# Kernel tuning notes

Measured on AMD Instinct MI355X. Metric: run time of the kernel, lower is better.

The kernel has to match this reference:

```python
import jax, jax.numpy as jnp
import numpy as np

D_MODEL = 1024
N_HEADS = 16
HEAD_DIM = D_MODEL // N_HEADS


def setup_inputs() -> dict:
    key = jax.random.key(0)
    ks = jax.random.split(key, 5)
    B, T = 2, 2048
    x = jax.random.normal(ks[0], (B, T, D_MODEL), dtype=jnp.float32)
    s = 1.0 / np.sqrt(D_MODEL)
    qkv_w = jax.random.uniform(ks[1], (3 * D_MODEL, D_MODEL), jnp.float32, -s, s)
    qkv_b = jax.random.uniform(ks[2], (3 * D_MODEL,), jnp.float32, -s, s)
    out_w = jax.random.uniform(ks[3], (D_MODEL, D_MODEL), jnp.float32, -s, s)
    out_b = jax.random.uniform(ks[4], (D_MODEL,), jnp.float32, -s, s)
    return {"x": x, "qkv_w": qkv_w, "qkv_b": qkv_b, "out_w": out_w, "out_b": out_b}


def reference(x, qkv_w, qkv_b, out_w, out_b):
    B, T, _ = x.shape
    # qkv projection: [B,T,3*D]
    qkv = x @ qkv_w.T + qkv_b
    qkv = qkv.reshape(B, T, 3, N_HEADS, HEAD_DIM)
    qkv = jnp.transpose(qkv, (2, 0, 3, 1, 4))  # [3,B,H,T,Hd]
    q, k, v = qkv[0], qkv[1], qkv[2]
    scale = 1.0 / np.sqrt(HEAD_DIM)
    scores = jnp.einsum("bhqd,bhkd->bhqk", q, k) * scale  # [B,H,T,T]
    causal = jnp.tril(jnp.ones((T, T), dtype=bool))
    scores = jnp.where(causal, scores, -jnp.inf)
    weights = jax.nn.softmax(scores, axis=-1)
    # dropout in eval mode (identity)
    out = jnp.einsum("bhqk,bhkd->bhqd", weights, v)  # [B,H,T,Hd]
    out = jnp.transpose(out, (0, 2, 1, 3)).reshape(B, T, D_MODEL)
    return out @ out_w.T + out_b
```

## Files before the change

### kernel.cpp

```cpp
#include <hip/hip_runtime.h>
#include <hip/hip_bf16.h>


typedef __bf16 bf16;
typedef bf16 bf16x8 __attribute__((ext_vector_type(8)));
typedef bf16 bf16x4 __attribute__((ext_vector_type(4)));
typedef float f32x4 __attribute__((ext_vector_type(4)));

#define MFMA16(a, b, c) __builtin_amdgcn_mfma_f32_16x16x32_bf16((a), (b), (c), 0, 0, 0)

static constexpr int D_MODEL = 1024;
static constexpr int NH = 16;
static constexpr int HD = 64;
static constexpr int SEQ = 2048;
static constexpr int NB = 2;
static constexpr float QSCALE = 0.125f * 1.44269504088896340736f;

__device__ __forceinline__ bf16x8 cvt8(const float* p) {
    float4 u0 = *(const float4*)p;
    float4 u1 = *(const float4*)(p + 4);
    bf16x8 v = { (bf16)u0.x, (bf16)u0.y, (bf16)u0.z, (bf16)u0.w,
                 (bf16)u1.x, (bf16)u1.y, (bf16)u1.z, (bf16)u1.w };
    return v;
}

__device__ __forceinline__ void async16(const bf16* g, bf16* l) {
    __builtin_amdgcn_global_load_lds(
        (const __attribute__((address_space(1))) void*)g,
        (__attribute__((address_space(3))) void*)l, 16, 0, 0);
}

__global__ __launch_bounds__(256)
void k_cast(const float* __restrict__ in, bf16* __restrict__ out, int n8)
{
    int i = blockIdx.x * 256 + threadIdx.x;
    if (i < n8) *(bf16x8*)&out[(size_t)i * 8] = cvt8(&in[(size_t)i * 8]);
}

__global__ __launch_bounds__(256)
void k_qkv(const bf16* __restrict__ x, const bf16* __restrict__ w,
           const float* __restrict__ bias,
           bf16* __restrict__ Qb, bf16* __restrict__ Kb, bf16* __restrict__ VbT)
{
    __shared__ bf16 As[128 * 32];
    __shared__ bf16 Ws[128 * 32];

    const int tid  = threadIdx.x;
    const int wv   = tid >> 6;
    const int lane = tid & 63;
    const int lr   = lane & 15;
    const int lk   = lane >> 4;
    const int wm   = wv >> 1, wn = wv & 1;
    const int m0   = blockIdx.x * 128;
    const int n0   = blockIdx.y * 128;

    const int sRow = tid >> 2;
    const int sCol = (tid & 3) * 8;
    const int sOff = sRow * 32 + sCol;

    f32x4 acc[4][4] = {};

    for (int kt = 0; kt < 1024; kt += 32) {
        __syncthreads();
        async16(&x[(size_t)(m0 + sRow     ) * 1024 + kt + sCol], &As[sOff]);
        async16(&x[(size_t)(m0 + 64 + sRow) * 1024 + kt + sCol], &As[64 * 32 + sOff]);
        async16(&w[(size_t)(n0 + sRow     ) * 1024 + kt + sCol], &Ws[sOff]);
        async16(&w[(size_t)(n0 + 64 + sRow) * 1024 + kt + sCol], &Ws[64 * 32 + sOff]);
        __syncthreads();

        bf16x8 a[4], b[4];
        #pragma unroll
        for (int i = 0; i < 4; i++) {
            a[i] = *(const bf16x8*)&As[(wm * 64 + i * 16 + lr) * 32 + lk * 8];
            b[i] = *(const bf16x8*)&Ws[(wn * 64 + i * 16 + lr) * 32 + lk * 8];
        }
        #pragma unroll
        for (int i = 0; i < 4; i++)
            #pragma unroll
            for (int j = 0; j < 4; j++)
                acc[i][j] = MFMA16(a[i], b[j], acc[i][j]);
    }

    #pragma unroll
    for (int i = 0; i < 4; i++) {
        #pragma unroll
        for (int j = 0; j < 4; j++) {
            const int gm0 = m0 + wm * 64 + i * 16 + lk * 4;
            const int gn  = n0 + wn * 64 + j * 16 + lr;
            const int sel = gn >> 10;
            const int rem = gn & 1023;
            const int h   = rem >> 6;
            const int hd  = rem & 63;
            const int bb  = gm0 >> 11;
            const int t0  = gm0 & 2047;
            if (sel == 2) {
                bf16x4 p;
                #pragma unroll
                for (int r = 0; r < 4; r++) p[r] = (bf16)(acc[i][j][r] + bias[gn]);
                *(bf16x4*)&VbT[((size_t)(bb * NH + h) * HD + hd) * SEQ + t0] = p;
            } else {
                #pragma unroll
                for (int r = 0; r < 4; r++) {
                    float v = acc[i][j][r] + bias[gn];
                    size_t idx = ((size_t)(bb * NH + h) * SEQ + t0 + r) * HD + hd;
                    if (sel == 0) Qb[idx] = (bf16)(v * QSCALE);
                    else          Kb[idx] = (bf16)v;
                }
            }
        }
    }
}

__global__ __launch_bounds__(256)
void k_attn(const bf16* __restrict__ Qb, const bf16* __restrict__ Kb,
            const bf16* __restrict__ VbT, bf16* __restrict__ AO)
{
    __shared__ bf16 Ks[2][64 * 64];
    __shared__ bf16 Vt[2][64 * 64];
    __shared__ bf16 Ps[64 * 64];

    const int tid  = threadIdx.x;
    const int wv   = tid >> 6;
    const int lane = tid & 63;
    const int lr   = lane & 15;
    const int lk   = lane >> 4;
    const int bh   = blockIdx.y;
    const int qt   = ((bh >> 3) & 1) ? (31 - (int)blockIdx.x) : (int)blockIdx.x;

    const bf16* Qp  = Qb  + (size_t)bh * SEQ * HD;
    const bf16* Kp  = Kb  + (size_t)bh * SEQ * HD;
    const bf16* Vtp = VbT + (size_t)bh * HD * SEQ;

    const int qg = qt * 64 + wv * 16 + lr;

    bf16x8 qf[2];
    qf[0] = *(const bf16x8*)&Qp[(size_t)qg * HD +      lk * 8];
    qf[1] = *(const bf16x8*)&Qp[(size_t)qg * HD + 32 + lk * 8];

    f32x4 ot[4] = {};
    float lsum = 0.f;

    const int srow   = tid >> 3;
    const int sgcol  = ((tid & 7) ^ (srow & 7)) * 8;
    const int sldse  = tid * 8;
    const int swz    = lr & 7;

    auto stage = [&](int buf, int k0) {
        async16(&Kp [(size_t)(k0 + srow     ) * HD  + sgcol], &Ks[buf][       sldse]);
        async16(&Kp [(size_t)(k0 + 32 + srow) * HD  + sgcol], &Ks[buf][2048 + sldse]);
        async16(&Vtp[(size_t)(srow          ) * SEQ + k0 + sgcol], &Vt[buf][       sldse]);
        async16(&Vtp[(size_t)(32 + srow     ) * SEQ + k0 + sgcol], &Vt[buf][2048 + sldse]);
    };

    stage(0, 0);

    for (int kt = 0; kt <= qt; kt++) {
        const int p = kt & 1;
        if (kt < qt) {
            stage(p ^ 1, (kt + 1) * 64);
            asm volatile("s_waitcnt vmcnt(4)" ::: "memory");
        } else {
            asm volatile("s_waitcnt vmcnt(0)" ::: "memory");
        }
        __builtin_amdgcn_s_barrier();

        f32x4 s[4] = {};
        #pragma unroll
        for (int j = 0; j < 4; j++) {
            #pragma unroll
            for (int c = 0; c < 2; c++) {
                bf16x8 ka = *(const bf16x8*)
                    &Ks[p][(j * 16 + lr) * 64 + (((4 * c + lk) ^ swz) << 3)];
                s[j] = MFMA16(ka, qf[c], s[j]);
            }
        }

        const int k0 = kt * 64;
        const bool diag = (kt == qt);
        #pragma unroll
        for (int j = 0; j < 4; j++) {
            const int keyb = k0 + j * 16 + lk * 4;
            f32x4 pv;
            #pragma unroll
            for (int r = 0; r < 4; r++) {
                float e = __builtin_amdgcn_exp2f(s[j][r]);
                if (diag) e = (keyb + r > qg) ? 0.f : e;
                pv[r] = e;
            }
            s[j] = pv;
            lsum += (pv[0] + pv[1]) + (pv[2] + pv[3]);
        }

        #pragma unroll
        for (int j = 0; j < 4; j++) {
            bf16x4 p4 = { (bf16)s[j][0], (bf16)s[j][1], (bf16)s[j][2], (bf16)s[j][3] };
            *(bf16x4*)&Ps[(wv * 16 + lr) * 64 +
                          (((2 * j + (lk >> 1)) ^ swz) << 3) + ((lk & 1) << 2)] = p4;
        }

        #pragma unroll
        for (int c = 0; c < 2; c++) {
            bf16x8 pb = *(const bf16x8*)
                &Ps[(wv * 16 + lr) * 64 + (((4 * c + lk) ^ swz) << 3)];
            #pragma unroll
            for (int jh = 0; jh < 4; jh++) {
                bf16x8 va = *(const bf16x8*)
                    &Vt[p][(jh * 16 + lr) * 64 + (((4 * c + lk) ^ swz) << 3)];
                ot[jh] = MFMA16(va, pb, ot[jh]);
            }
        }

        asm volatile("" ::: "memory");
        __builtin_amdgcn_s_barrier();
    }

    lsum += __shfl_xor(lsum, 16);
    lsum += __shfl_xor(lsum, 32);

    const float inv = 1.0f / lsum;
    const int b_ = bh >> 4, h_ = bh & 15;
    const size_t base = ((size_t)(b_ * SEQ + qg)) * D_MODEL + h_ * HD;
    #pragma unroll
    for (int jh = 0; jh < 4; jh++) {
        bf16x4 o4 = { (bf16)(ot[jh][0] * inv), (bf16)(ot[jh][1] * inv),
                      (bf16)(ot[jh][2] * inv), (bf16)(ot[jh][3] * inv) };
        *(bf16x4*)&AO[base + jh * 16 + lk * 4] = o4;
    }
}

__global__ __launch_bounds__(256)
void k_oproj(const bf16* __restrict__ a_, const bf16* __restrict__ w,
             const float* __restrict__ bias, float* __restrict__ out)
{
    __shared__ bf16 As[128 * 32];
    __shared__ bf16 Ws[64 * 32];

    const int tid  = threadIdx.x;
    const int wv   = tid >> 6;
    const int lane = tid & 63;
    const int lr   = lane & 15;
    const int lk   = lane >> 4;
    const int wm   = wv >> 1, wn = wv & 1;
    const int m0   = blockIdx.x * 128;
    const int n0   = blockIdx.y * 64;

    const int sRow = tid >> 2;
    const int sCol = (tid & 3) * 8;
    const int sOff = sRow * 32 + sCol;

    f32x4 acc[4][2] = {};

    for (int kt = 0; kt < 1024; kt += 32) {
        __syncthreads();
        async16(&a_[(size_t)(m0 + sRow     ) * 1024 + kt + sCol], &As[sOff]);
        async16(&a_[(size_t)(m0 + 64 + sRow) * 1024 + kt + sCol], &As[64 * 32 + sOff]);
        async16(&w [(size_t)(n0 + sRow     ) * 1024 + kt + sCol], &Ws[sOff]);
        __syncthreads();

        bf16x8 a[4], b[2];
        #pragma unroll
        for (int i = 0; i < 4; i++)
            a[i] = *(const bf16x8*)&As[(wm * 64 + i * 16 + lr) * 32 + lk * 8];
        #pragma unroll
        for (int j = 0; j < 2; j++)
            b[j] = *(const bf16x8*)&Ws[(wn * 32 + j * 16 + lr) * 32 + lk * 8];
        #pragma unroll
        for (int i = 0; i < 4; i++)
            #pragma unroll
            for (int j = 0; j < 2; j++)
                acc[i][j] = MFMA16(a[i], b[j], acc[i][j]);
    }

    #pragma unroll
    for (int i = 0; i < 4; i++) {
        #pragma unroll
        for (int j = 0; j < 2; j++) {
            #pragma unroll
            for (int r = 0; r < 4; r++) {
                int gm = m0 + wm * 64 + i * 16 + lk * 4 + r;
                int gn = n0 + wn * 32 + j * 16 + lr;
                out[(size_t)gm * 1024 + gn] = acc[i][j][r] + bias[gn];
            }
        }
    }
}

extern "C" void kernel_launch(void* const* d_in, const int* in_sizes, int n_in,
                              void* d_out, int out_size, void* d_ws, size_t ws_size,
                              hipStream_t stream)
{
    const float* x     = (const float*)d_in[0];
    const float* qkv_w = (const float*)d_in[1];
    const float* qkv_b = (const float*)d_in[2];
    const float* out_w = (const float*)d_in[3];
    const float* out_b = (const float*)d_in[4];
    float* out = (float*)d_out;

    const size_t SZ = (size_t)NB * NH * SEQ * HD;
    bf16* Qb  = (bf16*)d_ws;
    bf16* Kb  = Qb + SZ;
    bf16* VbT = Kb + SZ;
    bf16* AO  = VbT + SZ;
    bf16* xb  = AO + SZ;
    bf16* wqb = xb + SZ;
    bf16* wob = wqb + (size_t)3 * D_MODEL * D_MODEL;

    hipLaunchKernelGGL(k_cast, dim3(2048), dim3(256), 0, stream, x,     xb,  524288);
    hipLaunchKernelGGL(k_cast, dim3(1536), dim3(256), 0, stream, qkv_w, wqb, 393216);
    hipLaunchKernelGGL(k_cast, dim3(512),  dim3(256), 0, stream, out_w, wob, 131072);

    hipLaunchKernelGGL(k_qkv, dim3(32, 24), dim3(256), 0, stream,
                       xb, wqb, qkv_b, Qb, Kb, VbT);
    hipLaunchKernelGGL(k_attn, dim3(32, 32), dim3(256), 0, stream,
                       Qb, Kb, VbT, AO);
    hipLaunchKernelGGL(k_oproj, dim3(32, 16), dim3(256), 0, stream,
                       AO, wob, out_b, out);
}
```

Before: 176.2 us.

## Double-buffer LDS tiles in QKV and output projection GEMMs

Both projection GEMMs now use two LDS buffers. The next K-slice is fetched with async global-to-LDS loads while MFMAs run on the current slice, and partial vmcnt waits let only the older loads drain. This is meant to hide global load latency that the previous load-sync-compute loop exposed. It doubles LDS use per block, which may reduce occupancy, and it relies on hand-placed waitcnt and barrier for correctness.

```diff
diff --git a/kernel.cpp b/kernel.cpp
--- a/kernel.cpp
+++ b/kernel.cpp
@@ -42,8 +42,8 @@
            const float* __restrict__ bias,
            bf16* __restrict__ Qb, bf16* __restrict__ Kb, bf16* __restrict__ VbT)
 {
-    __shared__ bf16 As[128 * 32];
-    __shared__ bf16 Ws[128 * 32];
+    __shared__ bf16 As[2][128 * 32];
+    __shared__ bf16 Ws[2][128 * 32];
 
     const int tid  = threadIdx.x;
     const int wv   = tid >> 6;
@@ -58,27 +58,41 @@
     const int sCol = (tid & 3) * 8;
     const int sOff = sRow * 32 + sCol;
 
+    auto stage = [&](int buf, int kt) {
+        async16(&x[(size_t)(m0 + sRow     ) * 1024 + kt + sCol], &As[buf][sOff]);
+        async16(&x[(size_t)(m0 + 64 + sRow) * 1024 + kt + sCol], &As[buf][64 * 32 + sOff]);
+        async16(&w[(size_t)(n0 + sRow     ) * 1024 + kt + sCol], &Ws[buf][sOff]);
+        async16(&w[(size_t)(n0 + 64 + sRow) * 1024 + kt + sCol], &Ws[buf][64 * 32 + sOff]);
+    };
+
     f32x4 acc[4][4] = {};
 
-    for (int kt = 0; kt < 1024; kt += 32) {
-        __syncthreads();
-        async16(&x[(size_t)(m0 + sRow     ) * 1024 + kt + sCol], &As[sOff]);
-        async16(&x[(size_t)(m0 + 64 + sRow) * 1024 + kt + sCol], &As[64 * 32 + sOff]);
-        async16(&w[(size_t)(n0 + sRow     ) * 1024 + kt + sCol], &Ws[sOff]);
-        async16(&w[(size_t)(n0 + 64 + sRow) * 1024 + kt + sCol], &Ws[64 * 32 + sOff]);
-        __syncthreads();
+    stage(0, 0);
+
+    for (int it = 0; it < 32; it++) {
+        const int p = it & 1;
+        if (it < 31) {
+            stage(p ^ 1, (it + 1) * 32);
+            asm volatile("s_waitcnt vmcnt(4)" ::: "memory");
+        } else {
+            asm volatile("s_waitcnt vmcnt(0)" ::: "memory");
+        }
+        __builtin_amdgcn_s_barrier();
 
         bf16x8 a[4], b[4];
         #pragma unroll
         for (int i = 0; i < 4; i++) {
-            a[i] = *(const bf16x8*)&As[(wm * 64 + i * 16 + lr) * 32 + lk * 8];
-            b[i] = *(const bf16x8*)&Ws[(wn * 64 + i * 16 + lr) * 32 + lk * 8];
+            a[i] = *(const bf16x8*)&As[p][(wm * 64 + i * 16 + lr) * 32 + lk * 8];
+            b[i] = *(const bf16x8*)&Ws[p][(wn * 64 + i * 16 + lr) * 32 + lk * 8];
         }
         #pragma unroll
         for (int i = 0; i < 4; i++)
             #pragma unroll
             for (int j = 0; j < 4; j++)
                 acc[i][j] = MFMA16(a[i], b[j], acc[i][j]);
+
+        asm volatile("" ::: "memory");
+        __builtin_amdgcn_s_barrier();
     }
 
     #pragma unroll
@@ -232,8 +246,8 @@
 void k_oproj(const bf16* __restrict__ a_, const bf16* __restrict__ w,
              const float* __restrict__ bias, float* __restrict__ out)
 {
-    __shared__ bf16 As[128 * 32];
-    __shared__ bf16 Ws[64 * 32];
+    __shared__ bf16 As[2][128 * 32];
+    __shared__ bf16 Ws[2][64 * 32];
 
     const int tid  = threadIdx.x;
     const int wv   = tid >> 6;
@@ -248,27 +262,41 @@
     const int sCol = (tid & 3) * 8;
     const int sOff = sRow * 32 + sCol;
 
+    auto stage = [&](int buf, int kt) {
+        async16(&a_[(size_t)(m0 + sRow     ) * 1024 + kt + sCol], &As[buf][sOff]);
+        async16(&a_[(size_t)(m0 + 64 + sRow) * 1024 + kt + sCol], &As[buf][64 * 32 + sOff]);
+        async16(&w [(size_t)(n0 + sRow     ) * 1024 + kt + sCol], &Ws[buf][sOff]);
+    };
+
     f32x4 acc[4][2] = {};
 
-    for (int kt = 0; kt < 1024; kt += 32) {
-        __syncthreads();
-        async16(&a_[(size_t)(m0 + sRow     ) * 1024 + kt + sCol], &As[sOff]);
-        async16(&a_[(size_t)(m0 + 64 + sRow) * 1024 + kt + sCol], &As[64 * 32 + sOff]);
-        async16(&w [(size_t)(n0 + sRow     ) * 1024 + kt + sCol], &Ws[sOff]);
-        __syncthreads();
+    stage(0, 0);
+
+    for (int it = 0; it < 32; it++) {
+        const int p = it & 1;
+        if (it < 31) {
+            stage(p ^ 1, (it + 1) * 32);
+            asm volatile("s_waitcnt vmcnt(3)" ::: "memory");
+        } else {
+            asm volatile("s_waitcnt vmcnt(0)" ::: "memory");
+        }
+        __builtin_amdgcn_s_barrier();
 
         bf16x8 a[4], b[2];
         #pragma unroll
         for (int i = 0; i < 4; i++)
-            a[i] = *(const bf16x8*)&As[(wm * 64 + i * 16 + lr) * 32 + lk * 8];
+            a[i] = *(const bf16x8*)&As[p][(wm * 64 + i * 16 + lr) * 32 + lk * 8];
         #pragma unroll
         for (int j = 0; j < 2; j++)
-            b[j] = *(const bf16x8*)&Ws[(wn * 32 + j * 16 + lr) * 32 + lk * 8];
+            b[j] = *(const bf16x8*)&Ws[p][(wn * 32 + j * 16 + lr) * 32 + lk * 8];
         #pragma unroll
         for (int i = 0; i < 4; i++)
             #pragma unroll
             for (int j = 0; j < 2; j++)
                 acc[i][j] = MFMA16(a[i], b[j], acc[i][j]);
+
+        asm volatile("" ::: "memory");
+        __builtin_amdgcn_s_barrier();
     }
 
     #pragma unroll
```

Measured after the change: 184.3 us. 1.05x slower.
